# Kernel tuning notes

Hardware: AMD Instinct MI355X
Metric: run time of the kernel (lower is better)

The kernel has to match this reference:

```python
import jax, jax.numpy as jnp
import numpy as np
from jax import lax

T, N, C, S = 160, 64, 6625, 25  # time, batch, classes (blank=0), max target len
NEG = -1e5  # effectively -inf in log-space, finite for stable grads


def setup_inputs() -> dict:
    key = jax.random.key(0)
    k1, k2, k3 = jax.random.split(key, 3)
    # x is passed straight to nn.CTCLoss as log_probs, so it is log-softmax output
    logits = jax.random.normal(k1, (T, N, C), dtype=jnp.float32)
    x = jax.nn.log_softmax(logits, axis=-1)
    label_idx = jax.random.randint(k2, (N, S), 1, C)          # labels in [1, C-1], blank=0
    sequence_length = jax.random.randint(k3, (N,), 5, S + 1)  # target lengths in [5, S]
    return {"x": x, "label_idx": label_idx, "sequence_length": sequence_length}


def _ctc_loss(log_probs, targets, target_lengths, blank=0):
    # log_probs: [T, N, C]; targets: [N, S] padded; target_lengths: [N]
    Tt, Nn, Cc = log_probs.shape
    Ss = targets.shape[1]
    L = 2 * Ss + 1  # extended target: blank, t1, blank, t2, ..., blank
    ext = jnp.full((Nn, L), blank, dtype=targets.dtype).at[:, 1::2].set(targets)
    # transition l-2 -> l allowed iff ext[l] != blank and ext[l] != ext[l-2]
    can_skip = jnp.concatenate(
        [jnp.zeros((Nn, 2), bool), ext[:, 2:] != ext[:, :-2]], axis=1
    ) & (ext != blank)

    bidx = jnp.arange(Nn)[:, None]
    e0 = log_probs[0][bidx, ext]  # [N, L] emission at t=0
    alpha0 = jnp.full((Nn, L), NEG, log_probs.dtype)
    alpha0 = alpha0.at[:, 0].set(e0[:, 0]).at[:, 1].set(e0[:, 1])

    def step(alpha, lp_t):
        e = lp_t[bidx, ext]  # [N, L]
        s1 = jnp.concatenate([jnp.full((Nn, 1), NEG, alpha.dtype), alpha[:, :-1]], axis=1)
        s2 = jnp.concatenate([jnp.full((Nn, 2), NEG, alpha.dtype), alpha[:, :-2]], axis=1)
        a = jnp.logaddexp(alpha, s1)
        a = jnp.where(can_skip, jnp.logaddexp(a, s2), a)
        return a + e, None

    alpha_T, _ = lax.scan(step, alpha0, log_probs[1:])
    bvec = jnp.arange(Nn)
    last = 2 * target_lengths  # final blank position; last-1 = final label position
    ll = jnp.logaddexp(alpha_T[bvec, last], alpha_T[bvec, last - 1])
    loss = -ll
    # torch reduction='mean': per-example loss divided by target length, then batch mean
    return jnp.mean(loss / target_lengths.astype(log_probs.dtype))


def reference(x, label_idx, sequence_length):
    # original module returns {'loss': loss}; we return the scalar loss
    return _ctc_loss(x, label_idx, sequence_length)
```

## Files before the change

### kernel.cpp

```cpp
#include <hip/hip_runtime.h>


constexpr int Tt = 160;
constexpr int Nn = 64;
constexpr int Cc = 6625;
constexpr int Ss = 25;
constexpr int Ll = 2 * Ss + 1;
constexpr float NEGV = -1e5f;

__global__ __launch_bounds__(256) void ctc_alpha_kernel(
    const float* __restrict__ x,
    const int* __restrict__ labels,
    const int* __restrict__ seqlen,
    float* __restrict__ partial)
{
    const int n   = blockIdx.x;
    const int tid = threadIdx.x;

    __shared__ int   clsS[32];
    __shared__ float eC[Tt][26];

    if (tid < 26) {
        clsS[tid] = (tid == 0) ? 0 : labels[n * Ss + (tid - 1)];
    }
    __syncthreads();

    const float* xb = x + (size_t)n * Cc;
    constexpr int TOTAL = Tt * 26;
    constexpr int ITERS = (TOTAL + 255) / 256;
    float vals[ITERS];
    #pragma unroll
    for (int it = 0; it < ITERS; ++it) {
        int i = tid + it * 256;
        if (i < TOTAL) {
            int t = i / 26;
            int j = i - t * 26;
            vals[it] = xb[(size_t)t * (Nn * Cc) + clsS[j]];
        }
    }
    #pragma unroll
    for (int it = 0; it < ITERS; ++it) {
        int i = tid + it * 256;
        if (i < TOTAL) {
            int t = i / 26;
            int j = i - t * 26;
            eC[t][j] = vals[it];
        }
    }
    __syncthreads();

    if (tid >= 64) return;
    const int l = tid;

    int jj = (l & 1) ? (1 + (l >> 1)) : 0;
    if (jj > 25) jj = 0;

    bool can_skip = false;
    if ((l & 1) && l >= 3 && jj >= 2) {
        can_skip = (clsS[jj] != clsS[jj - 1]);
    }

    float alpha = (l <= 1) ? eC[0][jj] : NEGV;

    float e_next = eC[1][jj];
    for (int t = 1; t < Tt; ++t) {
        float e = e_next;
        int tn = (t + 1 < Tt) ? (t + 1) : (Tt - 1);
        e_next = eC[tn][jj];

        float s1 = __shfl_up(alpha, 1);
        float s2 = __shfl_up(alpha, 2);
        if (l < 1) s1 = NEGV;
        if (l < 2 || !can_skip) s2 = NEGV;

        float m = fmaxf(fmaxf(alpha, s1), s2);
        float sum = __expf(alpha - m) + __expf(s1 - m) + __expf(s2 - m);
        alpha = m + __logf(sum) + e;
    }

    const int len  = seqlen[n];
    const int last = 2 * len;
    float aL   = __shfl(alpha, last);
    float aLm1 = __shfl(alpha, last - 1);
    if (l == 0) {
        float m  = fmaxf(aL, aLm1);
        float ll = m + log1pf(__expf(-fabsf(aL - aLm1)));
        partial[n] = -ll / (float)len;
    }
}

__global__ void ctc_reduce_kernel(const float* __restrict__ partial,
                                  float* __restrict__ out)
{
    float v = partial[threadIdx.x];
    #pragma unroll
    for (int off = 32; off > 0; off >>= 1) v += __shfl_down(v, off);
    if (threadIdx.x == 0) out[0] = v * (1.0f / Nn);
}

extern "C" void kernel_launch(void* const* d_in, const int* in_sizes, int n_in,
                              void* d_out, int out_size, void* d_ws, size_t ws_size,
                              hipStream_t stream) {
    const float* x      = (const float*)d_in[0];
    const int*   labels = (const int*)d_in[1];
    const int*   seqlen = (const int*)d_in[2];
    float* out     = (float*)d_out;
    float* partial = (float*)d_ws;

    ctc_alpha_kernel<<<Nn, 256, 0, stream>>>(x, labels, seqlen, partial);
    ctc_reduce_kernel<<<1, 64, 0, stream>>>(partial, out);
}
```

Before: 328.5 us.

## Load emissions straight into registers and use DPP lane shifts in recursion

Drops the LDS staging of emissions and the 256-thread block. Each of 64 lanes now gathers its own 160 emission values directly into a fully unrolled register array. The serial alpha recursion replaces __shfl_up (ds_bpermute through LDS) with DPP wave-shift-right moves, cutting per-step latency on the critical path. The can_skip test is also computed with DPP shifts. Risks include high register pressure from the 160-entry array, and possible lack of wave_shr DPP support on newer CDNA targets.

```diff
diff --git a/kernel.cpp b/kernel.cpp
--- a/kernel.cpp
+++ b/kernel.cpp
@@ -5,77 +5,51 @@
 constexpr int Nn = 64;
 constexpr int Cc = 6625;
 constexpr int Ss = 25;
-constexpr int Ll = 2 * Ss + 1;
 constexpr float NEGV = -1e5f;
 
-__global__ __launch_bounds__(256) void ctc_alpha_kernel(
+__device__ __forceinline__ float dpp_shr1(float x) {
+    return __int_as_float(__builtin_amdgcn_update_dpp(
+        0, __float_as_int(x), 0x138 , 0xF, 0xF, true));
+}
+
+__global__ __launch_bounds__(64) void ctc_alpha_kernel(
     const float* __restrict__ x,
     const int* __restrict__ labels,
     const int* __restrict__ seqlen,
     float* __restrict__ partial)
 {
-    const int n   = blockIdx.x;
-    const int tid = threadIdx.x;
-
-    __shared__ int   clsS[32];
-    __shared__ float eC[Tt][26];
-
-    if (tid < 26) {
-        clsS[tid] = (tid == 0) ? 0 : labels[n * Ss + (tid - 1)];
-    }
-    __syncthreads();
-
-    const float* xb = x + (size_t)n * Cc;
-    constexpr int TOTAL = Tt * 26;
-    constexpr int ITERS = (TOTAL + 255) / 256;
-    float vals[ITERS];
-    #pragma unroll
-    for (int it = 0; it < ITERS; ++it) {
-        int i = tid + it * 256;
-        if (i < TOTAL) {
-            int t = i / 26;
-            int j = i - t * 26;
-            vals[it] = xb[(size_t)t * (Nn * Cc) + clsS[j]];
-        }
-    }
-    #pragma unroll
-    for (int it = 0; it < ITERS; ++it) {
-        int i = tid + it * 256;
-        if (i < TOTAL) {
-            int t = i / 26;
-            int j = i - t * 26;
-            eC[t][j] = vals[it];
-        }
-    }
-    __syncthreads();
-
-    if (tid >= 64) return;
-    const int l = tid;
+    const int n = blockIdx.x;
+    const int l = threadIdx.x;
 
     int jj = (l & 1) ? (1 + (l >> 1)) : 0;
-    if (jj > 25) jj = 0;
+    if (jj > Ss) jj = 0;
+    int cls = 0;
+    if (jj >= 1) cls = labels[n * Ss + (jj - 1)];
 
-    bool can_skip = false;
-    if ((l & 1) && l >= 3 && jj >= 2) {
-        can_skip = (clsS[jj] != clsS[jj - 1]);
+    int c1 = __builtin_amdgcn_update_dpp(0, cls, 0x138, 0xF, 0xF, true);
+    int c2 = __builtin_amdgcn_update_dpp(0, c1,  0x138, 0xF, 0xF, true);
+    const bool can_skip = (l & 1) && (l >= 3) && (cls != c2);
+    const bool lane_ge1 = (l >= 1);
+
+    const size_t strideT = (size_t)Nn * Cc;
+    const float* xp = x + (size_t)n * Cc + cls;
+    float e[Tt];
+    #pragma unroll
+    for (int t = 0; t < Tt; ++t) {
+        e[t] = xp[(size_t)t * strideT];
     }
+    __builtin_amdgcn_sched_barrier(0);
 
-    float alpha = (l <= 1) ? eC[0][jj] : NEGV;
-
-    float e_next = eC[1][jj];
+    float alpha = (l <= 1) ? e[0] : NEGV;
+    #pragma unroll
     for (int t = 1; t < Tt; ++t) {
-        float e = e_next;
-        int tn = (t + 1 < Tt) ? (t + 1) : (Tt - 1);
-        e_next = eC[tn][jj];
-
-        float s1 = __shfl_up(alpha, 1);
-        float s2 = __shfl_up(alpha, 2);
-        if (l < 1) s1 = NEGV;
-        if (l < 2 || !can_skip) s2 = NEGV;
-
+        float s1 = dpp_shr1(alpha);
+        float s2 = dpp_shr1(s1);
+        if (!lane_ge1) s1 = NEGV;
+        if (!can_skip) s2 = NEGV;
         float m = fmaxf(fmaxf(alpha, s1), s2);
         float sum = __expf(alpha - m) + __expf(s1 - m) + __expf(s2 - m);
-        alpha = m + __logf(sum) + e;
+        alpha = m + __logf(sum) + e[t];
     }
 
     const int len  = seqlen[n];
@@ -107,6 +81,6 @@
     float* out     = (float*)d_out;
     float* partial = (float*)d_ws;
 
-    ctc_alpha_kernel<<<Nn, 256, 0, stream>>>(x, labels, seqlen, partial);
+    ctc_alpha_kernel<<<Nn, 64, 0, stream>>>(x, labels, seqlen, partial);
     ctc_reduce_kernel<<<1, 64, 0, stream>>>(partial, out);
 }
```

New measurement: 321.6 us. 2.1% less time.
